# Kernel optimization log

Hardware: AMD Instinct MI355X
Metric: run time of the kernel (lower is better)

## Reference

```python
import jax, jax.numpy as jnp
import numpy as np

B, L, V = 16, 2048, 64


def setup_inputs() -> dict:
    key = jax.random.key(0)
    k1, k2, k3, k4 = jax.random.split(key, 4)
    idx = jax.random.randint(k1, (B, L), 0, V)                      # tokens
    Wq_w = jax.random.normal(k2, (V, V), jnp.float32) * 0.02         # nn.Linear weight
    Wv_w = jax.random.normal(k3, (V, V), jnp.float32) * 0.02 + np.float32(np.e)  # Wv.weight (+e init)
    v_emb = jax.random.normal(k4, (L, 1), jnp.float32) * 0.02        # nn.Embedding(length, 1)
    return {"idx": idx, "Wq_w": Wq_w, "Wv_w": Wv_w, "v_emb": v_emb}


def reference(idx, Wq_w, Wv_w, v_emb):
    Lx = v_emb.shape[0]
    Vx = Wq_w.shape[0]
    # e = one_hot token embedding, [B, L, V]
    e = jax.nn.one_hot(idx, Vx, dtype=jnp.float32)
    i = jnp.arange(Lx)
    # pos[i, j] = max(i - j, 0); learned relative-position score table [L, L]
    pos = jnp.maximum(i[:, None] - i[None, :], 0)
    pos_embd = v_emb[pos, 0]
    causal = i[:, None] >= i[None, :]                                # tril mask
    # Attention block 1: scores are the learned position table (no QK^T)
    attn1 = jax.nn.softmax(jnp.where(causal, pos_embd, -jnp.inf), axis=-1)  # [L, L]
    l1 = jnp.einsum('ts,bsv->btv', attn1, e)                         # [B, L, V]
    # Attention block 2: Wq(e) @ l1^T, masked softmax, attn @ e * scalar
    q = jnp.einsum('btv,uv->btu', e, Wq_w)                           # F.linear: e @ Wq^T
    scores = jnp.einsum('btv,bsv->bts', q, l1)                       # [B, L, L]
    attn2 = jax.nn.softmax(jnp.where(causal, scores, -jnp.inf), axis=-1)
    l2 = jnp.einsum('bts,bsv->btv', attn2, e) * Wv_w[0, 0]           # logits [B, L, V]
    return l2
```

## Files before the change

kernel.cpp:

```cpp
#include <hip/hip_runtime.h>


#define LSEQ 2048
#define NB 16
#define NV 64
#define NC 32
#define NBLK 1024
#define BPB 64

typedef __attribute__((ext_vector_type(8))) short bf16x8;
typedef __attribute__((ext_vector_type(4))) float f32x4;

__device__ __forceinline__ unsigned short f2bf(float f) {
  unsigned int u = __float_as_uint(f);
  return (unsigned short)((u + 0x7FFFu + ((u >> 16) & 1u)) >> 16);
}

__device__ __forceinline__ void bb_arrive(unsigned int* cnt, unsigned int* flag) {
  __syncthreads();
  if (threadIdx.x == 0) {
    unsigned int old = __hip_atomic_fetch_add(cnt, 1u, __ATOMIC_RELAXED,
                                              __HIP_MEMORY_SCOPE_AGENT);
    if (old == BPB - 1u)
      __hip_atomic_store(flag, 1u, __ATOMIC_RELAXED, __HIP_MEMORY_SCOPE_AGENT);
  }
}
__device__ __forceinline__ void bb_wait(unsigned int* flag) {
  if (threadIdx.x == 0) {
    while (__hip_atomic_load(flag, __ATOMIC_RELAXED,
                             __HIP_MEMORY_SCOPE_AGENT) == 0u)
      __builtin_amdgcn_s_sleep(2);
  }
  __syncthreads();
}

__global__ __launch_bounds__(256, 4) void k_fused(
    const int* __restrict__ idx, const float* __restrict__ Wq,
    const float* __restrict__ Wv, const float* __restrict__ v_emb,
    float* __restrict__ P, float* __restrict__ out,
    unsigned int* __restrict__ bar) {
  union SMem {
    struct {
      unsigned short Wqb[64 * 65];
      unsigned short ro[2048];
      unsigned short GL0[2208];
      unsigned short GL1[2176];
      float red[16][64];
      float red2[16][64];
      float Spart[32];
      float swsum[4];
    } g;
    struct {
      float Hs[NC][65];
      float pl[4][64];
      unsigned long long mk[4][64];
    } s;
  };
  __shared__ SMem sm;

  const int bid = blockIdx.x;
  const int tid = threadIdx.x;
  const int w = tid >> 6;
  const int lane = tid & 63;
  const int b = bid >> 6;

  unsigned int* cntb  = bar +   0 + b * 32;
  unsigned int* flagb = bar + 512 + b * 32;

  const int bn = 63 - (bid & 63);
  const int n0 = bn * 32;
  const int quad = lane >> 4;
  const int lm = lane & 15;
  const int nsub = w & 1;
  const int kh = w >> 1;
  const int nbase = n0 + nsub * 16;

  {
#pragma unroll
    for (int u = 0; u < 16; ++u) {
      const int e = tid * 16 + u;
      sm.g.Wqb[(e >> 6) * 65 + (e & 63)] = f2bf(Wq[e]);
    }
#pragma unroll
    for (int j = 0; j < 8; ++j) {
      const int t = tid * 8 + j;
      sm.g.ro[2047 - t] = (unsigned short)(idx[b * LSEQ + t] * 65);
    }
    float ev[8], ps8[8];
    float tot = 0.f;
    const int t0 = tid * 8;
#pragma unroll
    for (int j = 0; j < 8; ++j) {
      const float e = expf(v_emb[t0 + j]);
      tot += e; ev[j] = e; ps8[j] = tot;
    }
    float ws = tot;
#pragma unroll
    for (int d = 1; d < 64; d <<= 1) {
      float up = __shfl_up(ws, d);
      if (lane >= d) ws += up;
    }
    if (lane == 63) sm.g.swsum[w] = ws;
    __syncthreads();
    float wbase = 0.f;
#pragma unroll
    for (int k = 0; k < 4; ++k) if (k < w) wbase += sm.g.swsum[k];
    const float base = wbase + (ws - tot);
#pragma unroll
    for (int j = 0; j < 8; ++j) {
      const int d = t0 + j;
      const float Sv = base + ps8[j];
      if ((unsigned)(d - n0) < 32u) sm.g.Spart[d - n0] = Sv;
      const unsigned short bv = f2bf(ev[j]);
      sm.g.GL0[d + 127] = bv;
      sm.g.GL1[d + 126] = bv;
    }
    if (tid < 31) sm.g.GL0[96 + tid] = 0;
    if (tid < 30) sm.g.GL1[96 + tid] = 0;
    if (tid == 0) { sm.g.GL0[2175] = 0; sm.g.GL1[2174] = 0; sm.g.GL1[2175] = 0; }
    __syncthreads();
  }
  const float sinv = 1.0f / sm.g.Spart[nsub * 16 + lm];

  {
    const int sbase = nbase + lm - 1920;
    const int kstart = 2048 - (n0 + 32);
    const int iters = bn + 1;

    f32x4 acc[4];
#pragma unroll
    for (int mt = 0; mt < 4; ++mt) acc[mt] = (f32x4){0.f, 0.f, 0.f, 0.f};

    union AF { unsigned short s[8]; bf16x8 v; };
    union BF { unsigned int u[4]; bf16x8 v; };
    AF a[3][4];
    BF bb[3];

#define LOAD_FRAGS(J_, SL) do {                                             \
    const int k_ = kstart + (kh + 2 * (J_)) * 32;                           \
    const int i0_ = k_ + quad * 8;                                          \
    unsigned short ro_[8];                                                  \
    *(uint4*)ro_ = *(const uint4*)&sm.g.ro[i0_];                            \
_Pragma("unroll")                                                           \
    for (int j_ = 0; j_ < 8; ++j_) {                                        \
      const int base_ = (int)ro_[j_] + lm;                                  \
      a[SL][0].s[j_] = sm.g.Wqb[base_ +  0];                                \
      a[SL][1].s[j_] = sm.g.Wqb[base_ + 16];                                \
      a[SL][2].s[j_] = sm.g.Wqb[base_ + 32];                                \
      a[SL][3].s[j_] = sm.g.Wqb[base_ + 48];                                \
    }                                                                       \
    const int s_ = sbase + k_ + quad * 8;                                   \
    const unsigned int* gb_ = (s_ & 1) ? (const unsigned int*)sm.g.GL1      \
                                       : (const unsigned int*)sm.g.GL0;     \
    const int off_ = s_ >> 1;                                               \
    bb[SL].u[0] = gb_[off_ + 0]; bb[SL].u[1] = gb_[off_ + 1];               \
    bb[SL].u[2] = gb_[off_ + 2]; bb[SL].u[3] = gb_[off_ + 3];               \
  } while (0)

#define MFMA4(SL) do {                                                      \
    acc[0] = __builtin_amdgcn_mfma_f32_16x16x32_bf16(a[SL][0].v, bb[SL].v, acc[0], 0, 0, 0); \
    acc[1] = __builtin_amdgcn_mfma_f32_16x16x32_bf16(a[SL][1].v, bb[SL].v, acc[1], 0, 0, 0); \
    acc[2] = __builtin_amdgcn_mfma_f32_16x16x32_bf16(a[SL][2].v, bb[SL].v, acc[2], 0, 0, 0); \
    acc[3] = __builtin_amdgcn_mfma_f32_16x16x32_bf16(a[SL][3].v, bb[SL].v, acc[3], 0, 0, 0); \
  } while (0)

    const int J = (iters > kh) ? ((iters - kh + 1) >> 1) : 0;
    if (J > 0) {
      LOAD_FRAGS(0, 0);
      if (J > 1) LOAD_FRAGS(1, 1);
      int j = 0;
      while (true) {
        if (j + 2 < J) LOAD_FRAGS(j + 2, 2);
        MFMA4(0);
        if (++j >= J) break;
        if (j + 2 < J) LOAD_FRAGS(j + 2, 0);
        MFMA4(1);
        if (++j >= J) break;
        if (j + 2 < J) LOAD_FRAGS(j + 2, 1);
        MFMA4(2);
        if (++j >= J) break;
      }
    }
#undef LOAD_FRAGS
#undef MFMA4

    if (kh == 1) {
      float (*rd)[64] = nsub ? sm.g.red2 : sm.g.red;
#pragma unroll
      for (int mt = 0; mt < 4; ++mt)
#pragma unroll
        for (int r = 0; r < 4; ++r) rd[mt * 4 + r][lane] = acc[mt][r];
    }
    __syncthreads();
    if (kh == 0) {
      float (*rd)[64] = nsub ? sm.g.red2 : sm.g.red;
#pragma unroll
      for (int mt = 0; mt < 4; ++mt)
#pragma unroll
        for (int r = 0; r < 4; ++r) acc[mt][r] += rd[mt * 4 + r][lane];

#pragma unroll
      for (int mt = 0; mt < 4; ++mt) {
#pragma unroll
        for (int r = 0; r < 4; ++r) {
          const int c = mt * 16 + quad * 4 + r;
          const float val = __expf(acc[mt][r] * sinv);
          __hip_atomic_store(&P[((size_t)(b * 64 + c)) * LSEQ + nbase + lm],
                             val, __ATOMIC_RELAXED, __HIP_MEMORY_SCOPE_AGENT);
        }
      }
    }
  }
  bb_arrive(cntb, flagb);

  {
    const int c = bid & 63;
    const int* __restrict__ irow = idx + b * LSEQ;
    int ii[8];
#pragma unroll
    for (int r = 0; r < 8; ++r)
      ii[r] = irow[(w * 8 + r) * 64 + lane];

    bb_wait(flagb);

    const float* __restrict__ prow = P + (size_t)bid * LSEQ;
    float p[8];
#pragma unroll
    for (int r = 0; r < 8; ++r)
      p[r] = __hip_atomic_load(prow + (w * 8 + r) * 64 + lane,
                               __ATOMIC_RELAXED, __HIP_MEMORY_SCOPE_AGENT);

    for (int i = tid; i < NC * 65; i += 256) ((float*)sm.s.Hs)[i] = 0.f;
    __syncthreads();
#pragma unroll
    for (int r = 0; r < 8; ++r) atomicAdd(&sm.s.Hs[w * 8 + r][ii[r]], p[r]);
    __syncthreads();

    const int hhalf = lane >> 5, l32 = lane & 31;
#pragma unroll
    for (int r = 0; r < 8; ++r) {
      const int v = w * 16 + r * 2 + hhalf;
      const float h = sm.s.Hs[l32][v];
      float x = h;
#pragma unroll
      for (int d = 1; d < 32; d <<= 1) {
        float up = __shfl_up(x, d, 32);
        if (l32 >= d) x += up;
      }
      sm.s.Hs[l32][v] = x - h;
    }
    __syncthreads();

    const float wv = Wv[0];
#pragma unroll
    for (int r = 0; r < 8; ++r) {
      const int ch = w * 8 + r;
      unsigned long long em = __ballot(ii[r] == c);
      if (em == 0ull) continue;
      sm.s.pl[w][lane] = p[r];
      sm.s.mk[w][lane] = 0ull;
      atomicOr(&sm.s.mk[w][ii[r]], 1ull << lane);
      float ps = p[r];
#pragma unroll
      for (int d = 1; d < 64; d <<= 1) {
        float up = __shfl_up(ps, d);
        if (lane >= d) ps += up;
      }
      const float hbase = sm.s.Hs[ch][lane];
      float zex = hbase;
#pragma unroll
      for (int d = 1; d < 64; d <<= 1) zex += __shfl_xor(zex, d);
      const unsigned long long myMask = sm.s.mk[w][lane];
      while (em) {
        const int srel = __builtin_ctzll(em);
        em &= em - 1;
        unsigned long long mm = myMask &
            ((srel == 63) ? ~0ull : ((1ull << (srel + 1)) - 1ull));
        float B = hbase;
        while (mm) { const int l = __builtin_ctzll(mm); mm &= mm - 1; B += sm.s.pl[w][l]; }
        const float z = zex + __shfl(ps, srel);
        out[((size_t)(b * LSEQ + ch * 64 + srel)) * 64 + lane] = wv * B / z;
      }
    }
  }
}

extern "C" void kernel_launch(void* const* d_in, const int* in_sizes, int n_in,
                              void* d_out, int out_size, void* d_ws, size_t ws_size,
                              hipStream_t stream) {
  const int* idx     = (const int*)d_in[0];
  const float* Wq    = (const float*)d_in[1];
  const float* Wv    = (const float*)d_in[2];
  const float* v_emb = (const float*)d_in[3];
  float* out = (float*)d_out;

  float* P = (float*)d_ws + LSEQ;
  unsigned int* bar = (unsigned int*)((char*)d_ws + (16u << 20));

  hipMemsetAsync(bar, 0, 8192, stream);

  k_fused<<<dim3(NBLK), dim3(256), 0, stream>>>(idx, Wq, Wv, v_emb, P, out,
                                                bar);
}
```

Baseline: 118.5 us.

## Split fused kernel into GEMM and scan-emit kernels, dropping the grid barrier

```diff
diff --git a/kernel.cpp b/kernel.cpp
--- a/kernel.cpp
+++ b/kernel.cpp
@@ -6,7 +6,6 @@
 #define NV 64
 #define NC 32
 #define NBLK 1024
-#define BPB 64
 
 typedef __attribute__((ext_vector_type(8))) short bf16x8;
 typedef __attribute__((ext_vector_type(4))) float f32x4;
@@ -16,45 +15,18 @@
   return (unsigned short)((u + 0x7FFFu + ((u >> 16) & 1u)) >> 16);
 }
 
-__device__ __forceinline__ void bb_arrive(unsigned int* cnt, unsigned int* flag) {
-  __syncthreads();
-  if (threadIdx.x == 0) {
-    unsigned int old = __hip_atomic_fetch_add(cnt, 1u, __ATOMIC_RELAXED,
-                                              __HIP_MEMORY_SCOPE_AGENT);
-    if (old == BPB - 1u)
-      __hip_atomic_store(flag, 1u, __ATOMIC_RELAXED, __HIP_MEMORY_SCOPE_AGENT);
-  }
-}
-__device__ __forceinline__ void bb_wait(unsigned int* flag) {
-  if (threadIdx.x == 0) {
-    while (__hip_atomic_load(flag, __ATOMIC_RELAXED,
-                             __HIP_MEMORY_SCOPE_AGENT) == 0u)
-      __builtin_amdgcn_s_sleep(2);
-  }
-  __syncthreads();
-}
-
-__global__ __launch_bounds__(256, 4) void k_fused(
+__global__ __launch_bounds__(256, 4) void k_gemm(
     const int* __restrict__ idx, const float* __restrict__ Wq,
-    const float* __restrict__ Wv, const float* __restrict__ v_emb,
-    float* __restrict__ P, float* __restrict__ out,
-    unsigned int* __restrict__ bar) {
-  union SMem {
-    struct {
-      unsigned short Wqb[64 * 65];
-      unsigned short ro[2048];
-      unsigned short GL0[2208];
-      unsigned short GL1[2176];
-      float red[16][64];
-      float red2[16][64];
-      float Spart[32];
-      float swsum[4];
-    } g;
-    struct {
-      float Hs[NC][65];
-      float pl[4][64];
-      unsigned long long mk[4][64];
-    } s;
+    const float* __restrict__ v_emb, float* __restrict__ P) {
+  struct SMem {
+    unsigned short Wqb[64 * 65];
+    unsigned short ro[2048];
+    unsigned short GL0[2208];
+    unsigned short GL1[2176];
+    float red[16][64];
+    float red2[16][64];
+    float Spart[32];
+    float swsum[4];
   };
   __shared__ SMem sm;
 
@@ -63,9 +35,6 @@
   const int w = tid >> 6;
   const int lane = tid & 63;
   const int b = bid >> 6;
-
-  unsigned int* cntb  = bar +   0 + b * 32;
-  unsigned int* flagb = bar + 512 + b * 32;
 
   const int bn = 63 - (bid & 63);
   const int n0 = bn * 32;
@@ -79,12 +48,12 @@
 #pragma unroll
     for (int u = 0; u < 16; ++u) {
       const int e = tid * 16 + u;
-      sm.g.Wqb[(e >> 6) * 65 + (e & 63)] = f2bf(Wq[e]);
+      sm.Wqb[(e >> 6) * 65 + (e & 63)] = f2bf(Wq[e]);
     }
 #pragma unroll
     for (int j = 0; j < 8; ++j) {
       const int t = tid * 8 + j;
-      sm.g.ro[2047 - t] = (unsigned short)(idx[b * LSEQ + t] * 65);
+      sm.ro[2047 - t] = (unsigned short)(idx[b * LSEQ + t] * 65);
     }
     float ev[8], ps8[8];
     float tot = 0.f;
@@ -100,27 +69,27 @@
       float up = __shfl_up(ws, d);
       if (lane >= d) ws += up;
     }
-    if (lane == 63) sm.g.swsum[w] = ws;
+    if (lane == 63) sm.swsum[w] = ws;
     __syncthreads();
     float wbase = 0.f;
 #pragma unroll
-    for (int k = 0; k < 4; ++k) if (k < w) wbase += sm.g.swsum[k];
+    for (int k = 0; k < 4; ++k) if (k < w) wbase += sm.swsum[k];
     const float base = wbase + (ws - tot);
 #pragma unroll
     for (int j = 0; j < 8; ++j) {
       const int d = t0 + j;
       const float Sv = base + ps8[j];
-      if ((unsigned)(d - n0) < 32u) sm.g.Spart[d - n0] = Sv;
+      if ((unsigned)(d - n0) < 32u) sm.Spart[d - n0] = Sv;
       const unsigned short bv = f2bf(ev[j]);
-      sm.g.GL0[d + 127] = bv;
-      sm.g.GL1[d + 126] = bv;
-    }
-    if (tid < 31) sm.g.GL0[96 + tid] = 0;
-    if (tid < 30) sm.g.GL1[96 + tid] = 0;
-    if (tid == 0) { sm.g.GL0[2175] = 0; sm.g.GL1[2174] = 0; sm.g.GL1[2175] = 0; }
+      sm.GL0[d + 127] = bv;
+      sm.GL1[d + 126] = bv;
+    }
+    if (tid < 31) sm.GL0[96 + tid] = 0;
+    if (tid < 30) sm.GL1[96 + tid] = 0;
+    if (tid == 0) { sm.GL0[2175] = 0; sm.GL1[2174] = 0; sm.GL1[2175] = 0; }
     __syncthreads();
   }
-  const float sinv = 1.0f / sm.g.Spart[nsub * 16 + lm];
+  const float sinv = 1.0f / sm.Spart[nsub * 16 + lm];
 
   {
     const int sbase = nbase + lm - 1920;
@@ -140,18 +109,18 @@
     const int k_ = kstart + (kh + 2 * (J_)) * 32;                           \
     const int i0_ = k_ + quad * 8;                                          \
     unsigned short ro_[8];                                                  \
-    *(uint4*)ro_ = *(const uint4*)&sm.g.ro[i0_];                            \
+    *(uint4*)ro_ = *(const uint4*)&sm.ro[i0_];                              \
 _Pragma("unroll")                                                           \
     for (int j_ = 0; j_ < 8; ++j_) {                                        \
       const int base_ = (int)ro_[j_] + lm;                                  \
-      a[SL][0].s[j_] = sm.g.Wqb[base_ +  0];                                \
-      a[SL][1].s[j_] = sm.g.Wqb[base_ + 16];                                \
-      a[SL][2].s[j_] = sm.g.Wqb[base_ + 32];                                \
-      a[SL][3].s[j_] = sm.g.Wqb[base_ + 48];                                \
+      a[SL][0].s[j_] = sm.Wqb[base_ +  0];                                  \
+      a[SL][1].s[j_] = sm.Wqb[base_ + 16];                                  \
+      a[SL][2].s[j_] = sm.Wqb[base_ + 32];                                  \
+      a[SL][3].s[j_] = sm.Wqb[base_ + 48];                                  \
     }                                                                       \
     const int s_ = sbase + k_ + quad * 8;                                   \
-    const unsigned int* gb_ = (s_ & 1) ? (const unsigned int*)sm.g.GL1      \
-                                       : (const unsigned int*)sm.g.GL0;     \
+    const unsigned int* gb_ = (s_ & 1) ? (const unsigned int*)sm.GL1        \
+                                       : (const unsigned int*)sm.GL0;       \
     const int off_ = s_ >> 1;                                               \
     bb[SL].u[0] = gb_[off_ + 0]; bb[SL].u[1] = gb_[off_ + 1];               \
     bb[SL].u[2] = gb_[off_ + 2]; bb[SL].u[3] = gb_[off_ + 3];               \
@@ -185,7 +154,7 @@
 #undef MFMA4
 
     if (kh == 1) {
-      float (*rd)[64] = nsub ? sm.g.red2 : sm.g.red;
+      float (*rd)[64] = nsub ? sm.red2 : sm.red;
 #pragma unroll
       for (int mt = 0; mt < 4; ++mt)
 #pragma unroll
@@ -193,7 +162,7 @@
     }
     __syncthreads();
     if (kh == 0) {
-      float (*rd)[64] = nsub ? sm.g.red2 : sm.g.red;
+      float (*rd)[64] = nsub ? sm.red2 : sm.red;
 #pragma unroll
       for (int mt = 0; mt < 4; ++mt)
 #pragma unroll
@@ -204,83 +173,87 @@
 #pragma unroll
         for (int r = 0; r < 4; ++r) {
           const int c = mt * 16 + quad * 4 + r;
-          const float val = __expf(acc[mt][r] * sinv);
-          __hip_atomic_store(&P[((size_t)(b * 64 + c)) * LSEQ + nbase + lm],
-                             val, __ATOMIC_RELAXED, __HIP_MEMORY_SCOPE_AGENT);
+          P[((size_t)(b * 64 + c)) * LSEQ + nbase + lm] = __expf(acc[mt][r] * sinv);
         }
       }
     }
   }
-  bb_arrive(cntb, flagb);
-
-  {
-    const int c = bid & 63;
-    const int* __restrict__ irow = idx + b * LSEQ;
-    int ii[8];
-#pragma unroll
-    for (int r = 0; r < 8; ++r)
-      ii[r] = irow[(w * 8 + r) * 64 + lane];
-
-    bb_wait(flagb);
-
-    const float* __restrict__ prow = P + (size_t)bid * LSEQ;
-    float p[8];
-#pragma unroll
-    for (int r = 0; r < 8; ++r)
-      p[r] = __hip_atomic_load(prow + (w * 8 + r) * 64 + lane,
-                               __ATOMIC_RELAXED, __HIP_MEMORY_SCOPE_AGENT);
-
-    for (int i = tid; i < NC * 65; i += 256) ((float*)sm.s.Hs)[i] = 0.f;
-    __syncthreads();
-#pragma unroll
-    for (int r = 0; r < 8; ++r) atomicAdd(&sm.s.Hs[w * 8 + r][ii[r]], p[r]);
-    __syncthreads();
-
-    const int hhalf = lane >> 5, l32 = lane & 31;
-#pragma unroll
-    for (int r = 0; r < 8; ++r) {
-      const int v = w * 16 + r * 2 + hhalf;
-      const float h = sm.s.Hs[l32][v];
-      float x = h;
-#pragma unroll
-      for (int d = 1; d < 32; d <<= 1) {
-        float up = __shfl_up(x, d, 32);
-        if (l32 >= d) x += up;
-      }
-      sm.s.Hs[l32][v] = x - h;
-    }
-    __syncthreads();
-
-    const float wv = Wv[0];
-#pragma unroll
-    for (int r = 0; r < 8; ++r) {
-      const int ch = w * 8 + r;
-      unsigned long long em = __ballot(ii[r] == c);
-      if (em == 0ull) continue;
-      sm.s.pl[w][lane] = p[r];
-      sm.s.mk[w][lane] = 0ull;
-      atomicOr(&sm.s.mk[w][ii[r]], 1ull << lane);
-      float ps = p[r];
-#pragma unroll
-      for (int d = 1; d < 64; d <<= 1) {
-        float up = __shfl_up(ps, d);
-        if (lane >= d) ps += up;
-      }
-      const float hbase = sm.s.Hs[ch][lane];
-      float zex = hbase;
-#pragma unroll
-      for (int d = 1; d < 64; d <<= 1) zex += __shfl_xor(zex, d);
-      const unsigned long long myMask = sm.s.mk[w][lane];
-      while (em) {
-        const int srel = __builtin_ctzll(em);
-        em &= em - 1;
-        unsigned long long mm = myMask &
-            ((srel == 63) ? ~0ull : ((1ull << (srel + 1)) - 1ull));
-        float B = hbase;
-        while (mm) { const int l = __builtin_ctzll(mm); mm &= mm - 1; B += sm.s.pl[w][l]; }
-        const float z = zex + __shfl(ps, srel);
-        out[((size_t)(b * LSEQ + ch * 64 + srel)) * 64 + lane] = wv * B / z;
-      }
+}
+
+__global__ __launch_bounds__(256, 8) void k_scanemit(
+    const int* __restrict__ idx, const float* __restrict__ P,
+    const float* __restrict__ Wv, float* __restrict__ out) {
+  __shared__ float Hs[NC][65];
+  __shared__ float pl[4][64];
+  __shared__ unsigned long long mk[4][64];
+
+  const int bc = blockIdx.x;
+  const int b = bc >> 6;
+  const int c = bc & 63;
+  const int w = threadIdx.x >> 6;
+  const int lane = threadIdx.x & 63;
+  const int tid = threadIdx.x;
+
+  const float* __restrict__ prow = P + (size_t)bc * LSEQ;
+  const int* __restrict__ irow = idx + b * LSEQ;
+
+  float p[8]; int ii[8];
+#pragma unroll
+  for (int r = 0; r < 8; ++r) {
+    const int ch = w * 8 + r;
+    p[r] = prow[ch * 64 + lane];
+    ii[r] = irow[ch * 64 + lane];
+  }
+  for (int i = tid; i < NC * 65; i += 256) ((float*)Hs)[i] = 0.f;
+  __syncthreads();
+#pragma unroll
+  for (int r = 0; r < 8; ++r) atomicAdd(&Hs[w * 8 + r][ii[r]], p[r]);
+  __syncthreads();
+
+  const int hhalf = lane >> 5, l32 = lane & 31;
+#pragma unroll
+  for (int r = 0; r < 8; ++r) {
+    const int v = w * 16 + r * 2 + hhalf;
+    const float h = Hs[l32][v];
+    float x = h;
+#pragma unroll
+    for (int d = 1; d < 32; d <<= 1) {
+      float up = __shfl_up(x, d, 32);
+      if (l32 >= d) x += up;
+    }
+    Hs[l32][v] = x - h;
+  }
+  __syncthreads();
+
+  const float wv = Wv[0];
+#pragma unroll
+  for (int r = 0; r < 8; ++r) {
+    const int ch = w * 8 + r;
+    unsigned long long em = __ballot(ii[r] == c);
+    if (em == 0ull) continue;
+    pl[w][lane] = p[r];
+    mk[w][lane] = 0ull;
+    atomicOr(&mk[w][ii[r]], 1ull << lane);
+    float ps = p[r];
+#pragma unroll
+    for (int d = 1; d < 64; d <<= 1) {
+      float up = __shfl_up(ps, d);
+      if (lane >= d) ps += up;
+    }
+    const float hbase = Hs[ch][lane];
+    float zex = hbase;
+#pragma unroll
+    for (int d = 1; d < 64; d <<= 1) zex += __shfl_xor(zex, d);
+    const unsigned long long myMask = mk[w][lane];
+    while (em) {
+      const int srel = __builtin_ctzll(em);
+      em &= em - 1;
+      unsigned long long mm = myMask &
+          ((srel == 63) ? ~0ull : ((1ull << (srel + 1)) - 1ull));
+      float B = hbase;
+      while (mm) { const int l = __builtin_ctzll(mm); mm &= mm - 1; B += pl[w][l]; }
+      const float z = zex + __shfl(ps, srel);
+      out[((size_t)(b * LSEQ + ch * 64 + srel)) * 64 + lane] = wv * B / z;
     }
   }
 }
@@ -295,10 +268,7 @@
   float* out = (float*)d_out;
 
   float* P = (float*)d_ws + LSEQ;
-  unsigned int* bar = (unsigned int*)((char*)d_ws + (16u << 20));
-
-  hipMemsetAsync(bar, 0, 8192, stream);
-
-  k_fused<<<dim3(NBLK), dim3(256), 0, stream>>>(idx, Wq, Wv, v_emb, P, out,
-                                                bar);
-}
+
+  k_gemm<<<dim3(NBLK), dim3(256), 0, stream>>>(idx, Wq, v_emb, P);
+  k_scanemit<<<dim3(NBLK), dim3(256), 0, stream>>>(idx, P, Wv, out);
+}
```

Result: no change. 117.5 us (-0.9%).
